# Performance work log

Hardware: AMD Instinct MI355X
Metric: run time of the kernel (lower is better)

Reference implementation:

```python
import jax, jax.numpy as jnp
import numpy as np

B, S, F, H, O = 256, 512, 64, 1024, 24  # batch, seq_len, input_size, hidden_size, output_size


def setup_inputs() -> dict:
    key = jax.random.key(0)
    ks = jax.random.split(key, 11)
    s = 1.0 / np.sqrt(H)  # PyTorch LSTM/Linear uniform init bound
    u = lambda k, shape: jax.random.uniform(k, shape, jnp.float32, -s, s)
    return {
        "x": jax.random.normal(ks[0], (B, S, F), jnp.float32),
        # layer 0 (gate order: i, f, g, o stacked along first dim)
        "W_ih0": u(ks[1], (4 * H, F)),
        "W_hh0": u(ks[2], (4 * H, H)),
        "b_ih0": u(ks[3], (4 * H,)),
        "b_hh0": u(ks[4], (4 * H,)),
        # layer 1
        "W_ih1": u(ks[5], (4 * H, H)),
        "W_hh1": u(ks[6], (4 * H, H)),
        "b_ih1": u(ks[7], (4 * H,)),
        "b_hh1": u(ks[8], (4 * H,)),
        # final projection over all timesteps: [O, H*S]
        "fc_W": jax.random.uniform(ks[9], (O, H * S), jnp.float32, -1.0 / np.sqrt(H * S), 1.0 / np.sqrt(H * S)),
        "fc_b": jax.random.uniform(ks[10], (O,), jnp.float32, -1.0 / np.sqrt(H * S), 1.0 / np.sqrt(H * S)),
    }


def _lstm_layer(x_sbf, W_ih, W_hh, b_ih, b_hh):
    # x_sbf: [S, B, Fin]; returns all hidden states [S, B, H]
    Hh = W_hh.shape[1]
    # precompute input contribution for all steps (one big GEMM)
    xg = jnp.einsum('sbf,gf->sbg', x_sbf, W_ih) + b_ih + b_hh  # [S, B, 4H]

    def step(carry, xg_t):
        h, c = carry
        gates = xg_t + h @ W_hh.T  # [B, 4H]
        i, f, g, o = jnp.split(gates, 4, axis=-1)
        c = jax.nn.sigmoid(f) * c + jax.nn.sigmoid(i) * jnp.tanh(g)
        h = jax.nn.sigmoid(o) * jnp.tanh(c)
        return (h, c), h

    h0 = jnp.zeros((x_sbf.shape[1], Hh), x_sbf.dtype)
    _, hs = jax.lax.scan(step, (h0, h0), xg)
    return hs  # [S, B, H]


def reference(x, W_ih0, W_hh0, b_ih0, b_hh0, W_ih1, W_hh1, b_ih1, b_hh1, fc_W, fc_b):
    xs = jnp.swapaxes(x, 0, 1)  # [S, B, F]
    h1 = _lstm_layer(xs, W_ih0, W_hh0, b_ih0, b_hh0)  # [S, B, H]
    h2 = _lstm_layer(h1, W_ih1, W_hh1, b_ih1, b_hh1)  # [S, B, H]
    # use_all_h=True: reshape [B, S, H] -> [B, S*H], then Linear
    flat = jnp.swapaxes(h2, 0, 1).reshape(x.shape[0], -1)
    return flat @ fc_W.T + fc_b  # [B, O]
```

## Files before the change

kernel.cpp:

```cpp
#include <hip/hip_runtime.h>
#include <hip/hip_fp16.h>

#define B_ 256
#define S_ 512
#define F_ 64
#define H_ 1024
#define O_ 24
#define G_ 4096

typedef _Float16 half_t;
typedef _Float16 h8 __attribute__((ext_vector_type(8)));
typedef float f4 __attribute__((ext_vector_type(4)));

#define OFF_H1 ((size_t)0)
#define OFF_H2 (OFF_H1 + (size_t)2*B_*H_*2)
#define OFF_C1 (OFF_H2 + (size_t)2*B_*H_*2)
#define OFF_C2 (OFF_C1 + (size_t)B_*H_*4)
#define OFF_OP (OFF_C2 + (size_t)B_*H_*4)
#define ZBYTES (OFF_OP + (size_t)32*B_*O_*4)
#define OFF_BIAS0 (ZBYTES)
#define OFF_BIAS1 (OFF_BIAS0 + (size_t)G_*4)
#define OFF_XH    (OFF_BIAS1 + (size_t)G_*4)
#define OFF_WIH0  (OFF_XH + (size_t)B_*S_*F_*2)
#define OFF_WHH0  (OFF_WIH0 + (size_t)G_*F_*2)
#define OFF_WIH1  (OFF_WHH0 + (size_t)G_*H_*2)
#define OFF_WHH1  (OFF_WIH1 + (size_t)G_*H_*2)
#define WS_NEEDED (OFF_WHH1 + (size_t)G_*H_*2)

__global__ void k_bias(const float* __restrict__ bi0, const float* __restrict__ bh0,
                       const float* __restrict__ bi1, const float* __restrict__ bh1,
                       float* __restrict__ bias0, float* __restrict__ bias1) {
    int i = blockIdx.x * blockDim.x + threadIdx.x;
    if (i < G_) { bias0[i] = bi0[i] + bh0[i]; bias1[i] = bi1[i] + bh1[i]; }
}

__global__ void k_cvt(const float* __restrict__ src, half_t* __restrict__ dst, int n) {
    int i = blockIdx.x * blockDim.x + threadIdx.x;
    int stride = gridDim.x * blockDim.x;
    for (; i < n; i += stride) dst[i] = (half_t)src[i];
}

__global__ void k_pack(const float* __restrict__ src, half_t* __restrict__ dst, int NC) {
    int i = blockIdx.x * blockDim.x + threadIdx.x;
    int total = 32768 * NC;
    if (i >= total) return;
    int lane = i & 63;
    int j    = (i >> 6) & 3;
    int ck   = (i >> 8) % NC;
    int gh   = i / (256 * NC);
    int srow = (gh >> 5) * H_ + (gh & 31) * 32 + (j >> 1) * 16 + (lane & 15);
    int scol = ck * 64 + (j & 1) * 32 + (lane >> 4) * 8;
    const float* s = src + (size_t)srow * (NC * 64) + scol;
    h8 v;
    #pragma unroll
    for (int e = 0; e < 8; ++e) v[e] = (half_t)s[e];
    *(h8*)&dst[(size_t)i * 8] = v;
}

__global__ __launch_bounds__(256, 2)
void k_phase(int t,
             const half_t* __restrict__ x_h,
             const half_t* __restrict__ Wih0, const half_t* __restrict__ Whh0,
             const float* __restrict__ bias0, float* __restrict__ c1g, half_t* __restrict__ h1buf,
             const half_t* __restrict__ Wih1, const half_t* __restrict__ Whh1,
             const float* __restrict__ bias1, float* __restrict__ c2g, half_t* __restrict__ h2buf,
             const float* __restrict__ fcW, float* __restrict__ out_part)
{
    __shared__ __align__(16) char smraw[36864];
    half_t* A_s    = (half_t*)smraw;
    float*  gate_s = (float*)smraw;
    float*  h_s    = (float*)(smraw + 16896);

    const int n  = blockIdx.x;
    const bool l1 = (n < 256);
    const int m  = l1 ? n : n - 256;
    const int ht = (m & 7) + 8 * ((m >> 3) & 3);
    const int bt = (m >> 5) & 7;

    int tt; const half_t* xb; int ldx, cx; const half_t* Wih;
    const half_t* Whh; const float* bias; float* c; half_t* hn_out; const half_t* hp;
    if (l1) {
        if (t == 0) return;
        tt = t - 1;
        xb  = h1buf + (size_t)(tt & 1) * B_ * H_;  ldx = H_;      cx = 16;
        Wih = Wih1;  Whh = Whh1;  bias = bias1;  c = c2g;
        hp     = h2buf + (size_t)((tt - 1) & 1) * B_ * H_;
        hn_out = h2buf + (size_t)(tt & 1) * B_ * H_;
    } else {
        if (t >= S_) return;
        tt = t;
        xb  = x_h + (size_t)tt * F_;  ldx = S_ * F_;  cx = 1;
        Wih = Wih0;  Whh = Whh0;  bias = bias0;  c = c1g;
        hp     = h1buf + (size_t)((tt - 1) & 1) * B_ * H_;
        hn_out = h1buf + (size_t)(tt & 1) * B_ * H_;
    }

    const int thr  = threadIdx.x;
    const int wave = thr >> 6, lane = thr & 63;
    const int quad = lane >> 4, l15 = lane & 15;
    const int hbase = ht * 32;

    float bv0 = bias[wave * H_ + hbase + l15];
    float bv1 = bias[wave * H_ + hbase + 16 + l15];
    f4 acc[2][2];
    #pragma unroll
    for (int mt = 0; mt < 2; ++mt) {
        acc[mt][0] = (f4){bv0, bv0, bv0, bv0};
        acc[mt][1] = (f4){bv1, bv1, bv1, bv1};
    }

    const int nchunks = cx + 16;
    const int ghW = wave * 32 + ht;
    const int ar  = thr >> 3;
    const int ak  = (thr & 7) * 8;

    auto loadA = [&](int ck) -> f4 {
        const half_t* Ab; int lda, k0;
        if (ck < cx) { Ab = xb; lda = ldx; k0 = ck * 64; }
        else         { Ab = hp; lda = H_;  k0 = (ck - cx) * 64; }
        return *(const f4*)&Ab[(size_t)(bt * 32 + ar) * lda + k0 + ak];
    };
    auto fetchW = [&](int ck, h8& r0, h8& r1, h8& r2, h8& r3) {
        const half_t* Wb; int ckk, NC;
        if (ck < cx) { Wb = Wih; ckk = ck;      NC = cx; }
        else         { Wb = Whh; ckk = ck - cx; NC = 16; }
        const half_t* base = Wb + ((size_t)(((ghW * NC) + ckk) * 4) * 64 + lane) * 8;
        r0 = *(const h8*)(base + 0 * 512);
        r1 = *(const h8*)(base + 1 * 512);
        r2 = *(const h8*)(base + 2 * 512);
        r3 = *(const h8*)(base + 3 * 512);
    };

    for (int s = 0; s < nchunks; s += 8) {
        const int ns = (nchunks - s < 8) ? (nchunks - s) : 8;

        f4 p0, p1, p2, p3, p4, p5, p6, p7;
              p0 = loadA(s + 0);
        if (ns > 1)     p1 = loadA(s + 1);
        if (ns > 2)     p2 = loadA(s + 2);
        if (ns > 3)     p3 = loadA(s + 3);
        if (ns > 4)     p4 = loadA(s + 4);
        if (ns > 5)     p5 = loadA(s + 5);
        if (ns > 6)     p6 = loadA(s + 6);
        if (ns > 7)     p7 = loadA(s + 7);
        __syncthreads();
              *(f4*)&A_s[0 * 2304 + ar * 72 + ak] = p0;
        if (ns > 1)     *(f4*)&A_s[1 * 2304 + ar * 72 + ak] = p1;
        if (ns > 2)     *(f4*)&A_s[2 * 2304 + ar * 72 + ak] = p2;
        if (ns > 3)     *(f4*)&A_s[3 * 2304 + ar * 72 + ak] = p3;
        if (ns > 4)     *(f4*)&A_s[4 * 2304 + ar * 72 + ak] = p4;
        if (ns > 5)     *(f4*)&A_s[5 * 2304 + ar * 72 + ak] = p5;
        if (ns > 6)     *(f4*)&A_s[6 * 2304 + ar * 72 + ak] = p6;
        if (ns > 7)     *(f4*)&A_s[7 * 2304 + ar * 72 + ak] = p7;
        __syncthreads();

        h8 xw0, xw1, xw2, xw3, yw0, yw1, yw2, yw3;
        fetchW(s, xw0, xw1, xw2, xw3);

        #define STEP(i, C0,C1,C2,C3, N0,N1,N2,N3)                                              \
        if (i < ns) {                                                                          \
            if (i + 1 < ns) fetchW(s + i + 1, N0, N1, N2, N3);                                 \
            h8 a0 = *(const h8*)&A_s[i * 2304 + (0  + l15) * 72 + 0  + quad * 8];              \
            h8 a1 = *(const h8*)&A_s[i * 2304 + (16 + l15) * 72 + 0  + quad * 8];              \
            h8 a2 = *(const h8*)&A_s[i * 2304 + (0  + l15) * 72 + 32 + quad * 8];              \
            h8 a3 = *(const h8*)&A_s[i * 2304 + (16 + l15) * 72 + 32 + quad * 8];              \
            acc[0][0] = __builtin_amdgcn_mfma_f32_16x16x32_f16(a0, C0, acc[0][0], 0,0,0);      \
            acc[0][1] = __builtin_amdgcn_mfma_f32_16x16x32_f16(a0, C2, acc[0][1], 0,0,0);      \
            acc[1][0] = __builtin_amdgcn_mfma_f32_16x16x32_f16(a1, C0, acc[1][0], 0,0,0);      \
            acc[1][1] = __builtin_amdgcn_mfma_f32_16x16x32_f16(a1, C2, acc[1][1], 0,0,0);      \
            acc[0][0] = __builtin_amdgcn_mfma_f32_16x16x32_f16(a2, C1, acc[0][0], 0,0,0);      \
            acc[0][1] = __builtin_amdgcn_mfma_f32_16x16x32_f16(a2, C3, acc[0][1], 0,0,0);      \
            acc[1][0] = __builtin_amdgcn_mfma_f32_16x16x32_f16(a3, C1, acc[1][0], 0,0,0);      \
            acc[1][1] = __builtin_amdgcn_mfma_f32_16x16x32_f16(a3, C3, acc[1][1], 0,0,0);      \
        }
        STEP(0, xw0,xw1,xw2,xw3, yw0,yw1,yw2,yw3)
        STEP(1, yw0,yw1,yw2,yw3, xw0,xw1,xw2,xw3)
        STEP(2, xw0,xw1,xw2,xw3, yw0,yw1,yw2,yw3)
        STEP(3, yw0,yw1,yw2,yw3, xw0,xw1,xw2,xw3)
        STEP(4, xw0,xw1,xw2,xw3, yw0,yw1,yw2,yw3)
        STEP(5, yw0,yw1,yw2,yw3, xw0,xw1,xw2,xw3)
        STEP(6, xw0,xw1,xw2,xw3, yw0,yw1,yw2,yw3)
        STEP(7, yw0,yw1,yw2,yw3, xw0,xw1,xw2,xw3)
        #undef STEP
    }

    __syncthreads();

    #pragma unroll
    for (int mt = 0; mt < 2; ++mt)
        #pragma unroll
        for (int nt = 0; nt < 2; ++nt)
            #pragma unroll
            for (int r = 0; r < 4; ++r)
                gate_s[wave * (32 * 33) + (mt * 16 + quad * 4 + r) * 33 + nt * 16 + l15] = acc[mt][nt][r];
    __syncthreads();

    #pragma unroll
    for (int kk = 0; kk < 4; ++kk) {
        int e = thr + kk * 256;
        int b = e >> 5, col = e & 31;
        float gi = gate_s[0 * (32 * 33) + b * 33 + col];
        float gf = gate_s[1 * (32 * 33) + b * 33 + col];
        float gg = gate_s[2 * (32 * 33) + b * 33 + col];
        float go = gate_s[3 * (32 * 33) + b * 33 + col];
        float si = 1.f / (1.f + __expf(-gi));
        float sf = 1.f / (1.f + __expf(-gf));
        float so = 1.f / (1.f + __expf(-go));
        float tg = tanhf(gg);
        size_t cidx = (size_t)(bt * 32 + b) * H_ + hbase + col;
        float cn = sf * c[cidx] + si * tg;
        c[cidx] = cn;
        float hnv = so * tanhf(cn);
        hn_out[cidx] = (half_t)hnv;
        h_s[b * 33 + col] = hnv;
    }

    if (l1) {
        __syncthreads();
        const float* fcWt = fcW + (size_t)tt * H_;
        for (int p = thr; p < 32 * O_; p += 256) {
            int o = p >> 5, bb = p & 31;
            float s2 = 0.f;
            #pragma unroll 8
            for (int j = 0; j < 32; ++j)
                s2 += h_s[bb * 33 + j] * fcWt[(size_t)o * (S_ * H_) + hbase + j];
            out_part[ht * (B_ * O_) + (bt * 32 + bb) * O_ + o] += s2;
        }
    }
}

__global__ void k_final(const float* __restrict__ out_part, const float* __restrict__ fcb,
                        float* __restrict__ out) {
    int i = blockIdx.x * blockDim.x + threadIdx.x;
    if (i >= B_ * O_) return;
    int o = i % O_;
    float s = fcb[o];
    for (int t = 0; t < 32; ++t) s += out_part[t * (B_ * O_) + i];
    out[i] = s;
}

extern "C" void kernel_launch(void* const* d_in, const int* in_sizes, int n_in,
                              void* d_out, int out_size, void* d_ws, size_t ws_size,
                              hipStream_t stream) {
    const float* x    = (const float*)d_in[0];
    const float* Wih0 = (const float*)d_in[1];
    const float* Whh0 = (const float*)d_in[2];
    const float* bih0 = (const float*)d_in[3];
    const float* bhh0 = (const float*)d_in[4];
    const float* Wih1 = (const float*)d_in[5];
    const float* Whh1 = (const float*)d_in[6];
    const float* bih1 = (const float*)d_in[7];
    const float* bhh1 = (const float*)d_in[8];
    const float* fcW  = (const float*)d_in[9];
    const float* fcb  = (const float*)d_in[10];

    char* ws = (char*)d_ws;
    half_t* h1buf  = (half_t*)(ws + OFF_H1);
    half_t* h2buf  = (half_t*)(ws + OFF_H2);
    float*  c1     = (float*)(ws + OFF_C1);
    float*  c2     = (float*)(ws + OFF_C2);
    float*  opart  = (float*)(ws + OFF_OP);
    float*  bias0  = (float*)(ws + OFF_BIAS0);
    float*  bias1  = (float*)(ws + OFF_BIAS1);
    half_t* x_h    = (half_t*)(ws + OFF_XH);
    half_t* wih0_p = (half_t*)(ws + OFF_WIH0);
    half_t* whh0_p = (half_t*)(ws + OFF_WHH0);
    half_t* wih1_p = (half_t*)(ws + OFF_WIH1);
    half_t* whh1_p = (half_t*)(ws + OFF_WHH1);

    hipMemsetAsync(d_ws, 0, ZBYTES, stream);

    k_bias<<<dim3((G_ + 255) / 256), dim3(256), 0, stream>>>(bih0, bhh0, bih1, bhh1, bias0, bias1);
    k_cvt<<<dim3(2048), dim3(256), 0, stream>>>(x, x_h, B_ * S_ * F_);
    k_pack<<<dim3(128),  dim3(256), 0, stream>>>(Wih0, wih0_p, 1);
    k_pack<<<dim3(2048), dim3(256), 0, stream>>>(Whh0, whh0_p, 16);
    k_pack<<<dim3(2048), dim3(256), 0, stream>>>(Wih1, wih1_p, 16);
    k_pack<<<dim3(2048), dim3(256), 0, stream>>>(Whh1, whh1_p, 16);

    dim3 grid(512), blk(256);
    for (int t = 0; t <= S_; ++t) {
        k_phase<<<grid, blk, 0, stream>>>(t, x_h,
                                          wih0_p, whh0_p, bias0, c1, h1buf,
                                          wih1_p, whh1_p, bias1, c2, h2buf,
                                          fcW, opart);
    }
    k_final<<<dim3((B_ * O_ + 255) / 256), dim3(256), 0, stream>>>(opart, fcb, (float*)d_out);
}
```

Before: 10.63 ms.

## Double-buffer A tiles, deepen weight prefetch, and preload cell state and fc weights

```diff
diff --git a/kernel.cpp b/kernel.cpp
--- a/kernel.cpp
+++ b/kernel.cpp
@@ -66,10 +66,11 @@
              const float* __restrict__ bias1, float* __restrict__ c2g, half_t* __restrict__ h2buf,
              const float* __restrict__ fcW, float* __restrict__ out_part)
 {
-    __shared__ __align__(16) char smraw[36864];
+    __shared__ __align__(16) char smraw[73728];
     half_t* A_s    = (half_t*)smraw;
     float*  gate_s = (float*)smraw;
     float*  h_s    = (float*)(smraw + 16896);
+    float*  fcw_s  = (float*)(smraw + 21120);
 
     const int n  = blockIdx.x;
     const bool l1 = (n < 256);
@@ -131,39 +132,63 @@
         r3 = *(const h8*)(base + 3 * 512);
     };
 
+    h8 W0a,W0b,W0c,W0d, W1a,W1b,W1c,W1d, W2a,W2b,W2c,W2d, W3a,W3b,W3c,W3d;
+    f4 p0, p1, p2, p3, p4, p5, p6, p7;
+    p0 = loadA(0); p1 = loadA(1); p2 = loadA(2); p3 = loadA(3);
+    p4 = loadA(4); p5 = loadA(5); p6 = loadA(6); p7 = loadA(7);
+    fetchW(0, W0a,W0b,W0c,W0d);
+    fetchW(1, W1a,W1b,W1c,W1d);
+    fetchW(2, W2a,W2b,W2c,W2d);
+
+    float cpre[4];
+    #pragma unroll
+    for (int kk = 0; kk < 4; ++kk) {
+        int e = thr + kk * 256;
+        int b = e >> 5, col = e & 31;
+        cpre[kk] = c[(size_t)(bt * 32 + b) * H_ + hbase + col];
+    }
+    float fpre[3] = {0.f, 0.f, 0.f};
+    if (l1) {
+        const float* fcWt = fcW + (size_t)tt * H_;
+        #pragma unroll
+        for (int q = 0; q < 3; ++q) {
+            int p = thr + q * 256;
+            fpre[q] = fcWt[(size_t)(p >> 5) * (S_ * H_) + hbase + (p & 31)];
+        }
+    }
+
+    *(f4*)&A_s[0 * 2304 + ar * 72 + ak] = p0;
+    *(f4*)&A_s[1 * 2304 + ar * 72 + ak] = p1;
+    *(f4*)&A_s[2 * 2304 + ar * 72 + ak] = p2;
+    *(f4*)&A_s[3 * 2304 + ar * 72 + ak] = p3;
+    *(f4*)&A_s[4 * 2304 + ar * 72 + ak] = p4;
+    *(f4*)&A_s[5 * 2304 + ar * 72 + ak] = p5;
+    *(f4*)&A_s[6 * 2304 + ar * 72 + ak] = p6;
+    *(f4*)&A_s[7 * 2304 + ar * 72 + ak] = p7;
+    __syncthreads();
+
     for (int s = 0; s < nchunks; s += 8) {
-        const int ns = (nchunks - s < 8) ? (nchunks - s) : 8;
-
-        f4 p0, p1, p2, p3, p4, p5, p6, p7;
-              p0 = loadA(s + 0);
-        if (ns > 1)     p1 = loadA(s + 1);
-        if (ns > 2)     p2 = loadA(s + 2);
-        if (ns > 3)     p3 = loadA(s + 3);
-        if (ns > 4)     p4 = loadA(s + 4);
-        if (ns > 5)     p5 = loadA(s + 5);
-        if (ns > 6)     p6 = loadA(s + 6);
-        if (ns > 7)     p7 = loadA(s + 7);
-        __syncthreads();
-              *(f4*)&A_s[0 * 2304 + ar * 72 + ak] = p0;
-        if (ns > 1)     *(f4*)&A_s[1 * 2304 + ar * 72 + ak] = p1;
-        if (ns > 2)     *(f4*)&A_s[2 * 2304 + ar * 72 + ak] = p2;
-        if (ns > 3)     *(f4*)&A_s[3 * 2304 + ar * 72 + ak] = p3;
-        if (ns > 4)     *(f4*)&A_s[4 * 2304 + ar * 72 + ak] = p4;
-        if (ns > 5)     *(f4*)&A_s[5 * 2304 + ar * 72 + ak] = p5;
-        if (ns > 6)     *(f4*)&A_s[6 * 2304 + ar * 72 + ak] = p6;
-        if (ns > 7)     *(f4*)&A_s[7 * 2304 + ar * 72 + ak] = p7;
-        __syncthreads();
-
-        h8 xw0, xw1, xw2, xw3, yw0, yw1, yw2, yw3;
-        fetchW(s, xw0, xw1, xw2, xw3);
+        const int ns  = (nchunks - s < 8) ? (nchunks - s) : 8;
+        int ns2 = nchunks - s - 8; if (ns2 > 8) ns2 = 8;
+        const int bufo = ((s >> 3) & 1) * 18432;
+        const int obuf = 18432 - bufo;
+
+        if (ns2 > 0) p0 = loadA(s + 8 + 0);
+        if (ns2 > 1) p1 = loadA(s + 8 + 1);
+        if (ns2 > 2) p2 = loadA(s + 8 + 2);
+        if (ns2 > 3) p3 = loadA(s + 8 + 3);
+        if (ns2 > 4) p4 = loadA(s + 8 + 4);
+        if (ns2 > 5) p5 = loadA(s + 8 + 5);
+        if (ns2 > 6) p6 = loadA(s + 8 + 6);
+        if (ns2 > 7) p7 = loadA(s + 8 + 7);
 
         #define STEP(i, C0,C1,C2,C3, N0,N1,N2,N3)                                              \
         if (i < ns) {                                                                          \
-            if (i + 1 < ns) fetchW(s + i + 1, N0, N1, N2, N3);                                 \
-            h8 a0 = *(const h8*)&A_s[i * 2304 + (0  + l15) * 72 + 0  + quad * 8];              \
-            h8 a1 = *(const h8*)&A_s[i * 2304 + (16 + l15) * 72 + 0  + quad * 8];              \
-            h8 a2 = *(const h8*)&A_s[i * 2304 + (0  + l15) * 72 + 32 + quad * 8];              \
-            h8 a3 = *(const h8*)&A_s[i * 2304 + (16 + l15) * 72 + 32 + quad * 8];              \
+            if (s + i + 3 < nchunks) fetchW(s + i + 3, N0, N1, N2, N3);                        \
+            h8 a0 = *(const h8*)&A_s[bufo + i * 2304 + (0  + l15) * 72 + 0  + quad * 8];       \
+            h8 a1 = *(const h8*)&A_s[bufo + i * 2304 + (16 + l15) * 72 + 0  + quad * 8];       \
+            h8 a2 = *(const h8*)&A_s[bufo + i * 2304 + (0  + l15) * 72 + 32 + quad * 8];       \
+            h8 a3 = *(const h8*)&A_s[bufo + i * 2304 + (16 + l15) * 72 + 32 + quad * 8];       \
             acc[0][0] = __builtin_amdgcn_mfma_f32_16x16x32_f16(a0, C0, acc[0][0], 0,0,0);      \
             acc[0][1] = __builtin_amdgcn_mfma_f32_16x16x32_f16(a0, C2, acc[0][1], 0,0,0);      \
             acc[1][0] = __builtin_amdgcn_mfma_f32_16x16x32_f16(a1, C0, acc[1][0], 0,0,0);      \
@@ -173,15 +198,27 @@
             acc[1][0] = __builtin_amdgcn_mfma_f32_16x16x32_f16(a3, C1, acc[1][0], 0,0,0);      \
             acc[1][1] = __builtin_amdgcn_mfma_f32_16x16x32_f16(a3, C3, acc[1][1], 0,0,0);      \
         }
-        STEP(0, xw0,xw1,xw2,xw3, yw0,yw1,yw2,yw3)
-        STEP(1, yw0,yw1,yw2,yw3, xw0,xw1,xw2,xw3)
-        STEP(2, xw0,xw1,xw2,xw3, yw0,yw1,yw2,yw3)
-        STEP(3, yw0,yw1,yw2,yw3, xw0,xw1,xw2,xw3)
-        STEP(4, xw0,xw1,xw2,xw3, yw0,yw1,yw2,yw3)
-        STEP(5, yw0,yw1,yw2,yw3, xw0,xw1,xw2,xw3)
-        STEP(6, xw0,xw1,xw2,xw3, yw0,yw1,yw2,yw3)
-        STEP(7, yw0,yw1,yw2,yw3, xw0,xw1,xw2,xw3)
+        STEP(0, W0a,W0b,W0c,W0d,  W3a,W3b,W3c,W3d)
+        STEP(1, W1a,W1b,W1c,W1d,  W0a,W0b,W0c,W0d)
+        STEP(2, W2a,W2b,W2c,W2d,  W1a,W1b,W1c,W1d)
+        STEP(3, W3a,W3b,W3c,W3d,  W2a,W2b,W2c,W2d)
+        STEP(4, W0a,W0b,W0c,W0d,  W3a,W3b,W3c,W3d)
+        STEP(5, W1a,W1b,W1c,W1d,  W0a,W0b,W0c,W0d)
+        STEP(6, W2a,W2b,W2c,W2d,  W1a,W1b,W1c,W1d)
+        STEP(7, W3a,W3b,W3c,W3d,  W2a,W2b,W2c,W2d)
         #undef STEP
+
+        if (ns2 > 0) {
+                  *(f4*)&A_s[obuf + 0 * 2304 + ar * 72 + ak] = p0;
+            if (ns2 > 1)    *(f4*)&A_s[obuf + 1 * 2304 + ar * 72 + ak] = p1;
+            if (ns2 > 2)    *(f4*)&A_s[obuf + 2 * 2304 + ar * 72 + ak] = p2;
+            if (ns2 > 3)    *(f4*)&A_s[obuf + 3 * 2304 + ar * 72 + ak] = p3;
+            if (ns2 > 4)    *(f4*)&A_s[obuf + 4 * 2304 + ar * 72 + ak] = p4;
+            if (ns2 > 5)    *(f4*)&A_s[obuf + 5 * 2304 + ar * 72 + ak] = p5;
+            if (ns2 > 6)    *(f4*)&A_s[obuf + 6 * 2304 + ar * 72 + ak] = p6;
+            if (ns2 > 7)    *(f4*)&A_s[obuf + 7 * 2304 + ar * 72 + ak] = p7;
+            __syncthreads();
+        }
     }
 
     __syncthreads();
@@ -208,7 +245,7 @@
         float so = 1.f / (1.f + __expf(-go));
         float tg = tanhf(gg);
         size_t cidx = (size_t)(bt * 32 + b) * H_ + hbase + col;
-        float cn = sf * c[cidx] + si * tg;
+        float cn = sf * cpre[kk] + si * tg;
         c[cidx] = cn;
         float hnv = so * tanhf(cn);
         hn_out[cidx] = (half_t)hnv;
@@ -216,14 +253,16 @@
     }
 
     if (l1) {
+        fcw_s[thr]       = fpre[0];
+        fcw_s[thr + 256] = fpre[1];
+        fcw_s[thr + 512] = fpre[2];
         __syncthreads();
-        const float* fcWt = fcW + (size_t)tt * H_;
         for (int p = thr; p < 32 * O_; p += 256) {
             int o = p >> 5, bb = p & 31;
             float s2 = 0.f;
-            #pragma unroll 8
+            #pragma unroll
             for (int j = 0; j < 32; ++j)
-                s2 += h_s[bb * 33 + j] * fcWt[(size_t)o * (S_ * H_) + hbase + j];
+                s2 += h_s[bb * 33 + j] * fcw_s[o * 32 + j];
             out_part[ht * (B_ * O_) + (bt * 32 + bb) * O_ + o] += s2;
         }
     }
```

Measured after the change: 9.947 ms. -6.5%, faster.

## Retile LSTM phase kernel: 64x16 tiles, both layers per block, double-buffered A

Applied to the files above, without the earlier changes.

```diff
diff --git a/kernel.cpp b/kernel.cpp
--- a/kernel.cpp
+++ b/kernel.cpp
@@ -7,6 +7,7 @@
 #define H_ 1024
 #define O_ 24
 #define G_ 4096
+#define NT_ 64
 
 typedef _Float16 half_t;
 typedef _Float16 h8 __attribute__((ext_vector_type(8)));
@@ -17,7 +18,7 @@
 #define OFF_C1 (OFF_H2 + (size_t)2*B_*H_*2)
 #define OFF_C2 (OFF_C1 + (size_t)B_*H_*4)
 #define OFF_OP (OFF_C2 + (size_t)B_*H_*4)
-#define ZBYTES (OFF_OP + (size_t)32*B_*O_*4)
+#define ZBYTES (OFF_OP + (size_t)NT_*B_*O_*4)
 #define OFF_BIAS0 (ZBYTES)
 #define OFF_BIAS1 (OFF_BIAS0 + (size_t)G_*4)
 #define OFF_XH    (OFF_BIAS1 + (size_t)G_*4)
@@ -57,7 +58,150 @@
     *(h8*)&dst[(size_t)i * 8] = v;
 }
 
-__global__ __launch_bounds__(256, 2)
+__device__ __forceinline__ void run_part(
+    const int thr, const int bt, const int htp,
+    const int cx, const int nchunks,
+    const half_t* __restrict__ xb, const int ldx,
+    const half_t* __restrict__ hp,
+    const half_t* __restrict__ Wih, const half_t* __restrict__ Whh,
+    const float* __restrict__ bias,
+    float* __restrict__ c, half_t* __restrict__ hn_out,
+    const float* __restrict__ fcWt, float* __restrict__ out_part,
+    half_t* A_s, float* gate_s, float* h_s, float* fcw_s,
+    const bool do_fc)
+{
+    const int wave = thr >> 6, lane = thr & 63;
+    const int gate = wave >> 1, mh = wave & 1;
+    const int quad = lane >> 4, l15 = lane & 15;
+    const int ar = thr >> 3;
+    const int ak = (thr & 7) * 8;
+    const int ghW = gate * 32 + (htp >> 1);
+    const int jo  = (htp & 1) * 2;
+
+    float bv = bias[gate * H_ + htp * 16 + l15];
+    f4 acc0 = (f4){bv, bv, bv, bv};
+    f4 acc1 = acc0;
+
+    auto loadA = [&](int ck) -> f4 {
+        const half_t* Ab; int lda, k0;
+        if (ck < cx) { Ab = xb; lda = ldx; k0 = ck * 64; }
+        else         { Ab = hp; lda = H_;  k0 = (ck - cx) * 64; }
+        return *(const f4*)&Ab[(size_t)(bt * 64 + ar) * lda + k0 + ak];
+    };
+    auto fetchW = [&](int ck, h8& r0, h8& r1) {
+        const half_t* Wb; int ckk, NC;
+        if (ck < cx) { Wb = Wih; ckk = ck;      NC = cx; }
+        else         { Wb = Whh; ckk = ck - cx; NC = 16; }
+        const half_t* base = Wb + ((size_t)(((ghW * NC) + ckk) * 4 + jo) * 64 + lane) * 8;
+        r0 = *(const h8*)(base + 0 * 512);
+        r1 = *(const h8*)(base + 1 * 512);
+    };
+
+    h8 W0a,W0b, W1a,W1b, W2a,W2b, W3a,W3b;
+    f4 p0, p1, p2, p3;
+    p0 = loadA(0); p1 = loadA(1); p2 = loadA(2); p3 = loadA(3);
+    fetchW(0, W0a, W0b);
+    fetchW(1, W1a, W1b);
+    fetchW(2, W2a, W2b);
+
+    const int eb = thr >> 4, ecol = thr & 15;
+    const size_t cbase = (size_t)(bt * 64 + eb) * H_ + htp * 16 + ecol;
+    float cpre0 = c[cbase];
+    float cpre1 = c[cbase + (size_t)32 * H_];
+    float fpre = 0.f;
+    if (do_fc && thr < 384)
+        fpre = fcWt[(size_t)(thr >> 4) * (S_ * H_) + htp * 16 + (thr & 15)];
+
+    *(f4*)&A_s[0 * 4608 + ar * 72 + ak] = p0;
+    *(f4*)&A_s[1 * 4608 + ar * 72 + ak] = p1;
+    *(f4*)&A_s[2 * 4608 + ar * 72 + ak] = p2;
+    *(f4*)&A_s[3 * 4608 + ar * 72 + ak] = p3;
+    __syncthreads();
+
+    for (int s = 0; s < nchunks; s += 4) {
+        const int rem = nchunks - s;
+        const int ns = rem < 4 ? rem : 4;
+        int ns2 = rem - 4; if (ns2 < 0) ns2 = 0; if (ns2 > 4) ns2 = 4;
+        const int bufo = ((s >> 2) & 1) * 18432;
+        const int obuf = 18432 - bufo;
+
+        if (ns2 > 0) p0 = loadA(s + 4);
+        if (ns2 > 1) p1 = loadA(s + 5);
+        if (ns2 > 2) p2 = loadA(s + 6);
+        if (ns2 > 3) p3 = loadA(s + 7);
+
+        #define STEP(i, C0,C1, N0,N1)                                                          \
+        if (i < ns) {                                                                          \
+            if (s + i + 3 < nchunks) fetchW(s + i + 3, N0, N1);                                \
+            h8 a0 = *(const h8*)&A_s[bufo + i * 4608 + (mh * 32 + l15) * 72 + quad * 8];       \
+            h8 a1 = *(const h8*)&A_s[bufo + i * 4608 + (mh * 32 + 16 + l15) * 72 + quad * 8];  \
+            h8 a2 = *(const h8*)&A_s[bufo + i * 4608 + (mh * 32 + l15) * 72 + 32 + quad * 8];  \
+            h8 a3 = *(const h8*)&A_s[bufo + i * 4608 + (mh * 32 + 16 + l15) * 72 + 32 + quad * 8]; \
+            acc0 = __builtin_amdgcn_mfma_f32_16x16x32_f16(a0, C0, acc0, 0, 0, 0);              \
+            acc1 = __builtin_amdgcn_mfma_f32_16x16x32_f16(a1, C0, acc1, 0, 0, 0);              \
+            acc0 = __builtin_amdgcn_mfma_f32_16x16x32_f16(a2, C1, acc0, 0, 0, 0);              \
+            acc1 = __builtin_amdgcn_mfma_f32_16x16x32_f16(a3, C1, acc1, 0, 0, 0);              \
+        }
+        STEP(0, W0a,W0b, W3a,W3b)
+        STEP(1, W1a,W1b, W0a,W0b)
+        STEP(2, W2a,W2b, W1a,W1b)
+        STEP(3, W3a,W3b, W2a,W2b)
+        #undef STEP
+
+        if (ns2 > 0) {
+                   *(f4*)&A_s[obuf + 0 * 4608 + ar * 72 + ak] = p0;
+            if (ns2 > 1)     *(f4*)&A_s[obuf + 1 * 4608 + ar * 72 + ak] = p1;
+            if (ns2 > 2)     *(f4*)&A_s[obuf + 2 * 4608 + ar * 72 + ak] = p2;
+            if (ns2 > 3)     *(f4*)&A_s[obuf + 3 * 4608 + ar * 72 + ak] = p3;
+            __syncthreads();
+        }
+    }
+    __syncthreads();
+
+    #pragma unroll
+    for (int r = 0; r < 4; ++r) {
+        gate_s[gate * (64 * 17) + (mh * 32 + quad * 4 + r) * 17 + l15]      = acc0[r];
+        gate_s[gate * (64 * 17) + (mh * 32 + 16 + quad * 4 + r) * 17 + l15] = acc1[r];
+    }
+    __syncthreads();
+
+    #pragma unroll
+    for (int kk = 0; kk < 2; ++kk) {
+        int b = eb + kk * 32;
+        float gi = gate_s[0 * (64 * 17) + b * 17 + ecol];
+        float gf = gate_s[1 * (64 * 17) + b * 17 + ecol];
+        float gg = gate_s[2 * (64 * 17) + b * 17 + ecol];
+        float go = gate_s[3 * (64 * 17) + b * 17 + ecol];
+        float si = 1.f / (1.f + __expf(-gi));
+        float sf = 1.f / (1.f + __expf(-gf));
+        float so = 1.f / (1.f + __expf(-go));
+        float tg = tanhf(gg);
+        float cn = sf * (kk ? cpre1 : cpre0) + si * tg;
+        size_t cidx = cbase + (size_t)kk * 32 * H_;
+        c[cidx] = cn;
+        float hnv = so * tanhf(cn);
+        hn_out[cidx] = (half_t)hnv;
+        if (do_fc) h_s[b * 17 + ecol] = hnv;
+    }
+
+    if (do_fc) {
+        if (thr < 384) fcw_s[thr] = fpre;
+        __syncthreads();
+        #pragma unroll
+        for (int q = 0; q < 3; ++q) {
+            int p = thr + q * 512;
+            int o = p >> 6, bb = p & 63;
+            float s2 = 0.f;
+            #pragma unroll
+            for (int j = 0; j < 16; ++j)
+                s2 += h_s[bb * 17 + j] * fcw_s[o * 16 + j];
+            out_part[(size_t)htp * (B_ * O_) + (bt * 64 + bb) * O_ + o] += s2;
+        }
+    }
+    __syncthreads();
+}
+
+__global__ __launch_bounds__(512, 2)
 void k_phase(int t,
              const half_t* __restrict__ x_h,
              const half_t* __restrict__ Wih0, const half_t* __restrict__ Whh0,
@@ -66,166 +210,36 @@
              const float* __restrict__ bias1, float* __restrict__ c2g, half_t* __restrict__ h2buf,
              const float* __restrict__ fcW, float* __restrict__ out_part)
 {
-    __shared__ __align__(16) char smraw[36864];
+    __shared__ __align__(16) char smraw[73728];
     half_t* A_s    = (half_t*)smraw;
     float*  gate_s = (float*)smraw;
-    float*  h_s    = (float*)(smraw + 16896);
-
-    const int n  = blockIdx.x;
-    const bool l1 = (n < 256);
-    const int m  = l1 ? n : n - 256;
-    const int ht = (m & 7) + 8 * ((m >> 3) & 3);
-    const int bt = (m >> 5) & 7;
-
-    int tt; const half_t* xb; int ldx, cx; const half_t* Wih;
-    const half_t* Whh; const float* bias; float* c; half_t* hn_out; const half_t* hp;
-    if (l1) {
-        if (t == 0) return;
-        tt = t - 1;
-        xb  = h1buf + (size_t)(tt & 1) * B_ * H_;  ldx = H_;      cx = 16;
-        Wih = Wih1;  Whh = Whh1;  bias = bias1;  c = c2g;
-        hp     = h2buf + (size_t)((tt - 1) & 1) * B_ * H_;
-        hn_out = h2buf + (size_t)(tt & 1) * B_ * H_;
-    } else {
-        if (t >= S_) return;
-        tt = t;
-        xb  = x_h + (size_t)tt * F_;  ldx = S_ * F_;  cx = 1;
-        Wih = Wih0;  Whh = Whh0;  bias = bias0;  c = c1g;
-        hp     = h1buf + (size_t)((tt - 1) & 1) * B_ * H_;
-        hn_out = h1buf + (size_t)(tt & 1) * B_ * H_;
-    }
-
-    const int thr  = threadIdx.x;
-    const int wave = thr >> 6, lane = thr & 63;
-    const int quad = lane >> 4, l15 = lane & 15;
-    const int hbase = ht * 32;
-
-    float bv0 = bias[wave * H_ + hbase + l15];
-    float bv1 = bias[wave * H_ + hbase + 16 + l15];
-    f4 acc[2][2];
-    #pragma unroll
-    for (int mt = 0; mt < 2; ++mt) {
-        acc[mt][0] = (f4){bv0, bv0, bv0, bv0};
-        acc[mt][1] = (f4){bv1, bv1, bv1, bv1};
-    }
-
-    const int nchunks = cx + 16;
-    const int ghW = wave * 32 + ht;
-    const int ar  = thr >> 3;
-    const int ak  = (thr & 7) * 8;
-
-    auto loadA = [&](int ck) -> f4 {
-        const half_t* Ab; int lda, k0;
-        if (ck < cx) { Ab = xb; lda = ldx; k0 = ck * 64; }
-        else         { Ab = hp; lda = H_;  k0 = (ck - cx) * 64; }
-        return *(const f4*)&Ab[(size_t)(bt * 32 + ar) * lda + k0 + ak];
-    };
-    auto fetchW = [&](int ck, h8& r0, h8& r1, h8& r2, h8& r3) {
-        const half_t* Wb; int ckk, NC;
-        if (ck < cx) { Wb = Wih; ckk = ck;      NC = cx; }
-        else         { Wb = Whh; ckk = ck - cx; NC = 16; }
-        const half_t* base = Wb + ((size_t)(((ghW * NC) + ckk) * 4) * 64 + lane) * 8;
-        r0 = *(const h8*)(base + 0 * 512);
-        r1 = *(const h8*)(base + 1 * 512);
-        r2 = *(const h8*)(base + 2 * 512);
-        r3 = *(const h8*)(base + 3 * 512);
-    };
-
-    for (int s = 0; s < nchunks; s += 8) {
-        const int ns = (nchunks - s < 8) ? (nchunks - s) : 8;
-
-        f4 p0, p1, p2, p3, p4, p5, p6, p7;
-              p0 = loadA(s + 0);
-        if (ns > 1)     p1 = loadA(s + 1);
-        if (ns > 2)     p2 = loadA(s + 2);
-        if (ns > 3)     p3 = loadA(s + 3);
-        if (ns > 4)     p4 = loadA(s + 4);
-        if (ns > 5)     p5 = loadA(s + 5);
-        if (ns > 6)     p6 = loadA(s + 6);
-        if (ns > 7)     p7 = loadA(s + 7);
-        __syncthreads();
-              *(f4*)&A_s[0 * 2304 + ar * 72 + ak] = p0;
-        if (ns > 1)     *(f4*)&A_s[1 * 2304 + ar * 72 + ak] = p1;
-        if (ns > 2)     *(f4*)&A_s[2 * 2304 + ar * 72 + ak] = p2;
-        if (ns > 3)     *(f4*)&A_s[3 * 2304 + ar * 72 + ak] = p3;
-        if (ns > 4)     *(f4*)&A_s[4 * 2304 + ar * 72 + ak] = p4;
-        if (ns > 5)     *(f4*)&A_s[5 * 2304 + ar * 72 + ak] = p5;
-        if (ns > 6)     *(f4*)&A_s[6 * 2304 + ar * 72 + ak] = p6;
-        if (ns > 7)     *(f4*)&A_s[7 * 2304 + ar * 72 + ak] = p7;
-        __syncthreads();
-
-        h8 xw0, xw1, xw2, xw3, yw0, yw1, yw2, yw3;
-        fetchW(s, xw0, xw1, xw2, xw3);
-
-        #define STEP(i, C0,C1,C2,C3, N0,N1,N2,N3)                                              \
-        if (i < ns) {                                                                          \
-            if (i + 1 < ns) fetchW(s + i + 1, N0, N1, N2, N3);                                 \
-            h8 a0 = *(const h8*)&A_s[i * 2304 + (0  + l15) * 72 + 0  + quad * 8];              \
-            h8 a1 = *(const h8*)&A_s[i * 2304 + (16 + l15) * 72 + 0  + quad * 8];              \
-            h8 a2 = *(const h8*)&A_s[i * 2304 + (0  + l15) * 72 + 32 + quad * 8];              \
-            h8 a3 = *(const h8*)&A_s[i * 2304 + (16 + l15) * 72 + 32 + quad * 8];              \
-            acc[0][0] = __builtin_amdgcn_mfma_f32_16x16x32_f16(a0, C0, acc[0][0], 0,0,0);      \
-            acc[0][1] = __builtin_amdgcn_mfma_f32_16x16x32_f16(a0, C2, acc[0][1], 0,0,0);      \
-            acc[1][0] = __builtin_amdgcn_mfma_f32_16x16x32_f16(a1, C0, acc[1][0], 0,0,0);      \
-            acc[1][1] = __builtin_amdgcn_mfma_f32_16x16x32_f16(a1, C2, acc[1][1], 0,0,0);      \
-            acc[0][0] = __builtin_amdgcn_mfma_f32_16x16x32_f16(a2, C1, acc[0][0], 0,0,0);      \
-            acc[0][1] = __builtin_amdgcn_mfma_f32_16x16x32_f16(a2, C3, acc[0][1], 0,0,0);      \
-            acc[1][0] = __builtin_amdgcn_mfma_f32_16x16x32_f16(a3, C1, acc[1][0], 0,0,0);      \
-            acc[1][1] = __builtin_amdgcn_mfma_f32_16x16x32_f16(a3, C3, acc[1][1], 0,0,0);      \
-        }
-        STEP(0, xw0,xw1,xw2,xw3, yw0,yw1,yw2,yw3)
-        STEP(1, yw0,yw1,yw2,yw3, xw0,xw1,xw2,xw3)
-        STEP(2, xw0,xw1,xw2,xw3, yw0,yw1,yw2,yw3)
-        STEP(3, yw0,yw1,yw2,yw3, xw0,xw1,xw2,xw3)
-        STEP(4, xw0,xw1,xw2,xw3, yw0,yw1,yw2,yw3)
-        STEP(5, yw0,yw1,yw2,yw3, xw0,xw1,xw2,xw3)
-        STEP(6, xw0,xw1,xw2,xw3, yw0,yw1,yw2,yw3)
-        STEP(7, yw0,yw1,yw2,yw3, xw0,xw1,xw2,xw3)
-        #undef STEP
-    }
-
-    __syncthreads();
-
-    #pragma unroll
-    for (int mt = 0; mt < 2; ++mt)
-        #pragma unroll
-        for (int nt = 0; nt < 2; ++nt)
-            #pragma unroll
-            for (int r = 0; r < 4; ++r)
-                gate_s[wave * (32 * 33) + (mt * 16 + quad * 4 + r) * 33 + nt * 16 + l15] = acc[mt][nt][r];
-    __syncthreads();
-
-    #pragma unroll
-    for (int kk = 0; kk < 4; ++kk) {
-        int e = thr + kk * 256;
-        int b = e >> 5, col = e & 31;
-        float gi = gate_s[0 * (32 * 33) + b * 33 + col];
-        float gf = gate_s[1 * (32 * 33) + b * 33 + col];
-        float gg = gate_s[2 * (32 * 33) + b * 33 + col];
-        float go = gate_s[3 * (32 * 33) + b * 33 + col];
-        float si = 1.f / (1.f + __expf(-gi));
-        float sf = 1.f / (1.f + __expf(-gf));
-        float so = 1.f / (1.f + __expf(-go));
-        float tg = tanhf(gg);
-        size_t cidx = (size_t)(bt * 32 + b) * H_ + hbase + col;
-        float cn = sf * c[cidx] + si * tg;
-        c[cidx] = cn;
-        float hnv = so * tanhf(cn);
-        hn_out[cidx] = (half_t)hnv;
-        h_s[b * 33 + col] = hnv;
-    }
-
-    if (l1) {
-        __syncthreads();
-        const float* fcWt = fcW + (size_t)tt * H_;
-        for (int p = thr; p < 32 * O_; p += 256) {
-            int o = p >> 5, bb = p & 31;
-            float s2 = 0.f;
-            #pragma unroll 8
-            for (int j = 0; j < 32; ++j)
-                s2 += h_s[bb * 33 + j] * fcWt[(size_t)o * (S_ * H_) + hbase + j];
-            out_part[ht * (B_ * O_) + (bt * 32 + bb) * O_ + o] += s2;
-        }
+    float*  h_s    = (float*)(smraw + 17408);
+    float*  fcw_s  = (float*)(smraw + 21760);
+
+    const int n   = blockIdx.x;
+    const int htp = (n & 7) + 8 * ((n >> 3) & 7);
+    const int bt  = (n >> 6) & 3;
+    const int thr = threadIdx.x;
+
+    if (t < S_) {
+        const int tt = t;
+        run_part(thr, bt, htp, 1, 17,
+                 x_h + (size_t)tt * F_, S_ * F_,
+                 h1buf + (size_t)((tt - 1) & 1) * B_ * H_,
+                 Wih0, Whh0, bias0, c1g,
+                 h1buf + (size_t)(tt & 1) * B_ * H_,
+                 nullptr, nullptr,
+                 A_s, gate_s, h_s, fcw_s, false);
+    }
+    if (t > 0) {
+        const int tt = t - 1;
+        run_part(thr, bt, htp, 16, 32,
+                 h1buf + (size_t)(tt & 1) * B_ * H_, H_,
+                 h2buf + (size_t)((tt - 1) & 1) * B_ * H_,
+                 Wih1, Whh1, bias1, c2g,
+                 h2buf + (size_t)(tt & 1) * B_ * H_,
+                 fcW + (size_t)tt * H_, out_part,
+                 A_s, gate_s, h_s, fcw_s, true);
     }
 }
 
@@ -235,7 +249,7 @@
     if (i >= B_ * O_) return;
     int o = i % O_;
     float s = fcb[o];
-    for (int t = 0; t < 32; ++t) s += out_part[t * (B_ * O_) + i];
+    for (int tl = 0; tl < NT_; ++tl) s += out_part[(size_t)tl * (B_ * O_) + i];
     out[i] = s;
 }
 
@@ -277,7 +291,7 @@
     k_pack<<<dim3(2048), dim3(256), 0, stream>>>(Wih1, wih1_p, 16);
     k_pack<<<dim3(2048), dim3(256), 0, stream>>>(Whh1, whh1_p, 16);
 
-    dim3 grid(512), blk(256);
+    dim3 grid(256), blk(512);
     for (int t = 0; t <= S_; ++t) {
         k_phase<<<grid, blk, 0, stream>>>(t, x_h,
                                           wih0_p, whh0_p, bias0, c1, h1buf,
```

Measured after the change: 9.640 ms. 9.3% less time.
